# Optimization experiments

Hardware: AMD Instinct MI355X
Metric: run time of the kernel (lower is better)

The kernel has to match this reference:

```python
import jax, jax.numpy as jnp
import numpy as np

T, D = 8192, 1024      # num flattened tokens, hidden_dim
E, K = 8, 2            # n_experts, num_experts_per_tok


def setup_inputs() -> dict:
    key = jax.random.key(0)
    k1, k2, k3, k4, k5 = jax.random.split(key, 5)
    x = jax.random.normal(k1, (T, D), dtype=jnp.float32)
    flat_expert_indices = jax.random.randint(k2, (T * K,), 0, E, dtype=jnp.int32)
    flat_expert_weights = jax.random.uniform(k3, (T * K,), dtype=jnp.float32)
    # Expert params: fc1/fc2 are bias-free Linears, stored torch-style [out, in]
    W1 = jax.random.normal(k4, (E, D, D), dtype=jnp.float32) * (1.0 / np.sqrt(D))
    W2 = jax.random.normal(k5, (E, D, D), dtype=jnp.float32) * (1.0 / np.sqrt(D))
    return {"x": x, "flat_expert_indices": flat_expert_indices,
            "flat_expert_weights": flat_expert_weights, "W1": W1, "W2": W2}


def reference(x, flat_expert_indices, flat_expert_weights, W1, W2):
    # DummyExpert: relu(relu(x @ W1.T) @ W2.T), per expert (torch Linear = x @ W.T)
    # Dense dispatch: compute every expert on every token, then gather the
    # top-k expert outputs per token and combine with routing weights.
    h = jax.nn.relu(jnp.einsum('td,eod->eto', x, W1))   # [E, T, D]
    y = jax.nn.relu(jnp.einsum('eto,epo->etp', h, W2))  # [E, T, D]
    idx = flat_expert_indices.reshape(T, K)             # [T, K]
    w = flat_expert_weights.reshape(T, K)               # [T, K]
    yt = jnp.transpose(y, (1, 0, 2))                    # [T, E, D]
    sel = jnp.take_along_axis(yt, idx[:, :, None].astype(jnp.int32), axis=1)  # [T, K, D]
    return jnp.sum(sel * w[:, :, None], axis=1)         # [T, D]
```

## Files before the change

kernel.cpp:

```cpp
#include <hip/hip_runtime.h>

typedef unsigned short u16;
typedef unsigned int   u32;
typedef __attribute__((ext_vector_type(8))) short short8;
typedef __attribute__((ext_vector_type(4))) float f32x4;

#define T_TOK 8192
#define DIM   1024
#define NEXP  8
#define NPAIR (T_TOK * 2)

__device__ __forceinline__ u16 f2bf(float f) {
  u32 u = __builtin_bit_cast(u32, f);
  u32 r = (u + 0x7fffu + ((u >> 16) & 1u)) >> 16;
  return (u16)r;
}
__device__ __forceinline__ float bf2f(u16 b) {
  return __builtin_bit_cast(float, ((u32)b) << 16);
}

__device__ __forceinline__ void gl_lds16(const u16* g, u16* l) {
  __builtin_amdgcn_global_load_lds(
      (const __attribute__((address_space(1))) u32*)g,
      (__attribute__((address_space(3))) u32*)l,
      16, 0, 0);
}

__global__ void cast_bf16_k(const float* __restrict__ src, u16* __restrict__ dst, int n) {
  int i = (blockIdx.x * 256 + threadIdx.x) * 8;
  if (i >= n) return;
  f32x4 a = *(const f32x4*)(src + i);
  f32x4 b = *(const f32x4*)(src + i + 4);
  short8 o;
  o[0] = (short)f2bf(a[0]); o[1] = (short)f2bf(a[1]);
  o[2] = (short)f2bf(a[2]); o[3] = (short)f2bf(a[3]);
  o[4] = (short)f2bf(b[0]); o[5] = (short)f2bf(b[1]);
  o[6] = (short)f2bf(b[2]); o[7] = (short)f2bf(b[3]);
  *(short8*)(dst + i) = o;
}

__global__ void sort_pairs_k(const int* __restrict__ idx,
                             int* __restrict__ counts, int* __restrict__ offsets,
                             int* __restrict__ bucket, int* __restrict__ pos) {
  __shared__ int lc[NEXP], lo[NEXP], lcur[NEXP];
  const int tid = threadIdx.x;
  if (tid < NEXP) lc[tid] = 0;
  __syncthreads();
  for (int i = tid; i < NPAIR; i += 1024) atomicAdd(&lc[idx[i]], 1);
  __syncthreads();
  if (tid == 0) {
    int s = 0;
    for (int e = 0; e < NEXP; ++e) { lo[e] = s; lcur[e] = s; s += lc[e]; }
  }
  __syncthreads();
  for (int i = tid; i < NPAIR; i += 1024) {
    int e = idx[i];
    int p = atomicAdd(&lcur[e], 1);
    bucket[p] = i;
    pos[i] = p;
  }
  if (tid < NEXP) { counts[tid] = lc[tid]; offsets[tid] = lo[tid]; }
}

template <int GATHER>
__global__ __launch_bounds__(256, 2)
void moe_gemm_k(const u16* __restrict__ A,
                const u16* __restrict__ W,
                u16* __restrict__ O,
                const int* __restrict__ counts,
                const int* __restrict__ offsets,
                const int* __restrict__ bucket) {
  const int e   = blockIdx.z;
  const int cnt = counts[e];
  const int m0  = blockIdx.y << 7;
  if (m0 >= cnt) return;
  const int seg = offsets[e];
  const int n0  = blockIdx.x << 7;

  __shared__ u16 As[128 * 32];
  __shared__ u16 Bs[128 * 32];

  const int tid  = threadIdx.x;
  const int lane = tid & 63;
  const int wave = tid >> 6;

  int aoff[2], boff[2];
#pragma unroll
  for (int j = 0; j < 2; ++j) {
    const int c  = ((wave << 1) + j) * 64 + lane;
    const int r  = c >> 2;
    const int kc = (c & 3) << 3;
    int p = seg + m0 + r;
    p = (p < seg + cnt) ? p : (seg + cnt - 1);
    int rowbase;
    if (GATHER) { const int pair = bucket[p]; rowbase = (pair >> 1) * DIM; }
    else        { rowbase = p * DIM; }
    aoff[j] = rowbase + kc;
    boff[j] = e * DIM * DIM + (n0 + r) * DIM + kc;
  }

  f32x4 acc[4][4] = {};

  const int wm   = (wave >> 1) << 6;
  const int wn   = (wave & 1) << 6;
  const int lr   = lane & 15;
  const int quad = lane >> 4;

  for (int k0 = 0; k0 < DIM; k0 += 32) {
    __syncthreads();
#pragma unroll
    for (int j = 0; j < 2; ++j) {
      const int instr = (wave << 1) + j;
      gl_lds16(A + aoff[j] + k0, &As[instr << 9]);
      gl_lds16(W + boff[j] + k0, &Bs[instr << 9]);
    }
    __syncthreads();

    short8 af[4], bf[4];
#pragma unroll
    for (int mi = 0; mi < 4; ++mi)
      af[mi] = *(const short8*)&As[(wm + (mi << 4) + lr) * 32 + (quad << 3)];
#pragma unroll
    for (int ni = 0; ni < 4; ++ni)
      bf[ni] = *(const short8*)&Bs[(wn + (ni << 4) + lr) * 32 + (quad << 3)];
#pragma unroll
    for (int mi = 0; mi < 4; ++mi)
#pragma unroll
      for (int ni = 0; ni < 4; ++ni)
        acc[mi][ni] = __builtin_amdgcn_mfma_f32_16x16x32_bf16(af[mi], bf[ni], acc[mi][ni], 0, 0, 0);
  }

  const int pend = seg + cnt;
#pragma unroll
  for (int mi = 0; mi < 4; ++mi) {
#pragma unroll
    for (int ni = 0; ni < 4; ++ni) {
      const int col = n0 + wn + (ni << 4) + lr;
#pragma unroll
      for (int r4 = 0; r4 < 4; ++r4) {
        const int p = seg + m0 + wm + (mi << 4) + (quad << 2) + r4;
        if (p < pend) {
          float v = acc[mi][ni][r4];
          v = v > 0.f ? v : 0.f;
          O[(size_t)p * DIM + col] = f2bf(v);
        }
      }
    }
  }
}

__global__ void combine_k(const u16* __restrict__ y, const int* __restrict__ pos,
                          const float* __restrict__ wts, float* __restrict__ out) {
  const int t    = blockIdx.x * 2 + (threadIdx.x >> 7);
  const int lane = threadIdx.x & 127;
  const int col  = lane * 8;
  const int p0 = pos[2 * t], p1 = pos[2 * t + 1];
  const float w0 = wts[2 * t], w1 = wts[2 * t + 1];
  const short8 a = *(const short8*)(y + (size_t)p0 * DIM + col);
  const short8 b = *(const short8*)(y + (size_t)p1 * DIM + col);
  f32x4 o0, o1;
#pragma unroll
  for (int j = 0; j < 8; ++j) {
    float v = w0 * bf2f((u16)a[j]) + w1 * bf2f((u16)b[j]);
    if (j < 4) o0[j] = v; else o1[j - 4] = v;
  }
  float* op = out + (size_t)t * DIM + col;
  *(f32x4*)op = o0;
  *(f32x4*)(op + 4) = o1;
}

extern "C" void kernel_launch(void* const* d_in, const int* in_sizes, int n_in,
                              void* d_out, int out_size, void* d_ws, size_t ws_size,
                              hipStream_t stream) {
  const float* x   = (const float*)d_in[0];
  const int*   idx = (const int*)d_in[1];
  const float* wts = (const float*)d_in[2];
  const float* W1  = (const float*)d_in[3];
  const float* W2  = (const float*)d_in[4];
  float* out = (float*)d_out;

  char* ws = (char*)d_ws;
  int* counts  = (int*)ws;
  int* offsets = (int*)(ws + 32);
  int* bucket  = (int*)(ws + 256);
  int* pos     = (int*)(ws + 256 + 4 * NPAIR);
  const size_t base = 131328;
  const size_t MB16 = 16ull * 1024 * 1024;
  u16* xb  = (u16*)(ws + base);
  u16* w1b = (u16*)(ws + base + MB16);
  u16* w2b = (u16*)(ws + base + 2 * MB16);
  u16* h   = (u16*)(ws + base + 3 * MB16);
  u16* yb  = xb;

  const int nX = T_TOK * DIM;
  const int nW = NEXP * DIM * DIM;

  cast_bf16_k<<<nX / 2048, 256, 0, stream>>>(x, xb, nX);
  cast_bf16_k<<<nW / 2048, 256, 0, stream>>>(W1, w1b, nW);
  cast_bf16_k<<<nW / 2048, 256, 0, stream>>>(W2, w2b, nW);

  sort_pairs_k<<<1, 1024, 0, stream>>>(idx, counts, offsets, bucket, pos);

  dim3 gg(DIM / 128, NPAIR / 128, NEXP);
  moe_gemm_k<1><<<gg, 256, 0, stream>>>(xb, w1b, h, counts, offsets, bucket);
  moe_gemm_k<0><<<gg, 256, 0, stream>>>(h, w2b, yb, counts, offsets, bucket);

  combine_k<<<T_TOK / 2, 256, 0, stream>>>(yb, pos, wts, out);
}
```

Before: 294.4 us.

## Double-buffer GEMM LDS tiles, fuse casts, and use ballot-based expert sort

The MoE GEMM now double-buffers its A and B LDS tiles. The next k-slice is issued with global_load_lds before the current slice is consumed, leaving one barrier per iteration instead of two, so load latency can overlap MFMA work at the cost of twice the LDS. The three fp32-to-bf16 cast launches are merged into one kernel that picks its source and destination by region. The single-block pair sort replaces shared-memory atomics with per-wave ballot/popcount counting and ranking, which is deterministic.

```diff
diff --git a/kernel.cpp b/kernel.cpp
--- a/kernel.cpp
+++ b/kernel.cpp
@@ -2,6 +2,7 @@
 
 typedef unsigned short u16;
 typedef unsigned int   u32;
+typedef unsigned long long u64;
 typedef __attribute__((ext_vector_type(8))) short short8;
 typedef __attribute__((ext_vector_type(4))) float f32x4;
 
@@ -26,40 +27,82 @@
       16, 0, 0);
 }
 
-__global__ void cast_bf16_k(const float* __restrict__ src, u16* __restrict__ dst, int n) {
-  int i = (blockIdx.x * 256 + threadIdx.x) * 8;
-  if (i >= n) return;
-  f32x4 a = *(const f32x4*)(src + i);
-  f32x4 b = *(const f32x4*)(src + i + 4);
+__global__ void cast3_k(const float* __restrict__ x, const float* __restrict__ W1,
+                        const float* __restrict__ W2,
+                        u16* __restrict__ xb, u16* __restrict__ w1b, u16* __restrict__ w2b) {
+  const int g = (blockIdx.x * 256 + threadIdx.x) * 8;
+  const int region = g >> 23;
+  const int i = g & 0x7fffff;
+  const float* s = (region == 0) ? x : (region == 1) ? W1 : W2;
+  u16* d = (region == 0) ? xb : (region == 1) ? w1b : w2b;
+  f32x4 a = *(const f32x4*)(s + i);
+  f32x4 b = *(const f32x4*)(s + i + 4);
   short8 o;
   o[0] = (short)f2bf(a[0]); o[1] = (short)f2bf(a[1]);
   o[2] = (short)f2bf(a[2]); o[3] = (short)f2bf(a[3]);
   o[4] = (short)f2bf(b[0]); o[5] = (short)f2bf(b[1]);
   o[6] = (short)f2bf(b[2]); o[7] = (short)f2bf(b[3]);
-  *(short8*)(dst + i) = o;
+  *(short8*)(d + i) = o;
 }
 
 __global__ void sort_pairs_k(const int* __restrict__ idx,
                              int* __restrict__ counts, int* __restrict__ offsets,
                              int* __restrict__ bucket, int* __restrict__ pos) {
-  __shared__ int lc[NEXP], lo[NEXP], lcur[NEXP];
-  const int tid = threadIdx.x;
-  if (tid < NEXP) lc[tid] = 0;
+  __shared__ int lc[16][NEXP];
+  __shared__ int lo[16][NEXP];
+  const int tid  = threadIdx.x;
+  const int w    = tid >> 6;
+  const int lane = tid & 63;
+  const u64 ltmask = (lane == 63) ? 0x7fffffffffffffffull : ((1ull << lane) - 1);
+
+  int e_i[16];
+#pragma unroll
+  for (int i = 0; i < 16; ++i) e_i[i] = idx[(w * 16 + i) * 64 + lane];
+
+  int cnt[NEXP] = {};
+#pragma unroll
+  for (int i = 0; i < 16; ++i) {
+#pragma unroll
+    for (int ex = 0; ex < NEXP; ++ex) {
+      u64 m = __ballot(e_i[i] == ex);
+      cnt[ex] += (int)__popcll(m);
+    }
+  }
+  if (lane == 0) {
+#pragma unroll
+    for (int ex = 0; ex < NEXP; ++ex) lc[w][ex] = cnt[ex];
+  }
   __syncthreads();
-  for (int i = tid; i < NPAIR; i += 1024) atomicAdd(&lc[idx[i]], 1);
-  __syncthreads();
+
   if (tid == 0) {
     int s = 0;
-    for (int e = 0; e < NEXP; ++e) { lo[e] = s; lcur[e] = s; s += lc[e]; }
+    for (int ex = 0; ex < NEXP; ++ex) {
+      offsets[ex] = s;
+      int c = 0;
+      for (int ww = 0; ww < 16; ++ww) { lo[ww][ex] = s; s += lc[ww][ex]; c += lc[ww][ex]; }
+      counts[ex] = c;
+    }
   }
   __syncthreads();
-  for (int i = tid; i < NPAIR; i += 1024) {
-    int e = idx[i];
-    int p = atomicAdd(&lcur[e], 1);
-    bucket[p] = i;
-    pos[i] = p;
-  }
-  if (tid < NEXP) { counts[tid] = lc[tid]; offsets[tid] = lo[tid]; }
+
+  int cur[NEXP];
+#pragma unroll
+  for (int ex = 0; ex < NEXP; ++ex) cur[ex] = lo[w][ex];
+#pragma unroll
+  for (int i = 0; i < 16; ++i) {
+    const int item = (w * 16 + i) * 64 + lane;
+    const int e = e_i[i];
+    int p = 0;
+#pragma unroll
+    for (int ex = 0; ex < NEXP; ++ex) {
+      u64 m = __ballot(e == ex);
+      int rank = (int)__popcll(m & ltmask);
+      if (e == ex) p = cur[ex] + rank;
+      cur[ex] += (int)__popcll(m);
+    }
+    bucket[p] = item;
+    pos[item] = p;
+  }
 }
 
 template <int GATHER>
@@ -77,8 +120,8 @@
   const int seg = offsets[e];
   const int n0  = blockIdx.x << 7;
 
-  __shared__ u16 As[128 * 32];
-  __shared__ u16 Bs[128 * 32];
+  __shared__ u16 As[2][128 * 32];
+  __shared__ u16 Bs[2][128 * 32];
 
   const int tid  = threadIdx.x;
   const int lane = tid & 63;
@@ -106,23 +149,32 @@
   const int lr   = lane & 15;
   const int quad = lane >> 4;
 
+#pragma unroll
+  for (int j = 0; j < 2; ++j) {
+    const int instr = (wave << 1) + j;
+    gl_lds16(A + aoff[j], &As[0][instr << 9]);
+    gl_lds16(W + boff[j], &Bs[0][instr << 9]);
+  }
+
   for (int k0 = 0; k0 < DIM; k0 += 32) {
+    const int cur = (k0 >> 5) & 1;
     __syncthreads();
-#pragma unroll
-    for (int j = 0; j < 2; ++j) {
-      const int instr = (wave << 1) + j;
-      gl_lds16(A + aoff[j] + k0, &As[instr << 9]);
-      gl_lds16(W + boff[j] + k0, &Bs[instr << 9]);
-    }
-    __syncthreads();
+    if (k0 + 32 < DIM) {
+#pragma unroll
+      for (int j = 0; j < 2; ++j) {
+        const int instr = (wave << 1) + j;
+        gl_lds16(A + aoff[j] + k0 + 32, &As[cur ^ 1][instr << 9]);
+        gl_lds16(W + boff[j] + k0 + 32, &Bs[cur ^ 1][instr << 9]);
+      }
+    }
 
     short8 af[4], bf[4];
 #pragma unroll
     for (int mi = 0; mi < 4; ++mi)
-      af[mi] = *(const short8*)&As[(wm + (mi << 4) + lr) * 32 + (quad << 3)];
+      af[mi] = *(const short8*)&As[cur][(wm + (mi << 4) + lr) * 32 + (quad << 3)];
 #pragma unroll
     for (int ni = 0; ni < 4; ++ni)
-      bf[ni] = *(const short8*)&Bs[(wn + (ni << 4) + lr) * 32 + (quad << 3)];
+      bf[ni] = *(const short8*)&Bs[cur][(wn + (ni << 4) + lr) * 32 + (quad << 3)];
 #pragma unroll
     for (int mi = 0; mi < 4; ++mi)
 #pragma unroll
@@ -192,13 +244,7 @@
   u16* h   = (u16*)(ws + base + 3 * MB16);
   u16* yb  = xb;
 
-  const int nX = T_TOK * DIM;
-  const int nW = NEXP * DIM * DIM;
-
-  cast_bf16_k<<<nX / 2048, 256, 0, stream>>>(x, xb, nX);
-  cast_bf16_k<<<nW / 2048, 256, 0, stream>>>(W1, w1b, nW);
-  cast_bf16_k<<<nW / 2048, 256, 0, stream>>>(W2, w2b, nW);
-
+  cast3_k<<<3 * 4096, 256, 0, stream>>>(x, W1, W2, xb, w1b, w2b);
   sort_pairs_k<<<1, 1024, 0, stream>>>(idx, counts, offsets, bucket, pos);
 
   dim3 gg(DIM / 128, NPAIR / 128, NEXP);
```

Result: no change. 299.2 us (+1.6%).
